# Performance work log

Hardware: AMD Instinct MI355X
Metric: run time of the kernel (lower is better)

## Reference

```python
import jax, jax.numpy as jnp
import numpy as np

N = 50000      # nodes
E = 800000     # edges (before self-loops)
G = 64         # graphs in batch
IN, HID, OUT, H = 128, 64, 64, 4
NEG_SLOPE = 0.2
BN_EPS = 1e-5


def setup_inputs() -> dict:
    key = jax.random.key(0)
    ks = jax.random.split(key, 16)
    s = 0.1
    return {
        "x": jax.random.normal(ks[0], (N, IN), jnp.float32),
        "edge_index": jax.random.randint(ks[1], (2, E), 0, N, dtype=jnp.int64),
        "batch": jnp.sort(jax.random.randint(ks[2], (N,), 0, G, dtype=jnp.int64)),
        "num_graphs": G,
        "W1": jax.random.normal(ks[3], (IN, H * HID), jnp.float32) * s,
        "att_src1": jax.random.normal(ks[4], (H, HID), jnp.float32) * s,
        "att_dst1": jax.random.normal(ks[5], (H, HID), jnp.float32) * s,
        "b1": jnp.zeros((HID,), jnp.float32),
        "W2": jax.random.normal(ks[6], (HID, H * OUT), jnp.float32) * s,
        "att_src2": jax.random.normal(ks[7], (H, OUT), jnp.float32) * s,
        "att_dst2": jax.random.normal(ks[8], (H, OUT), jnp.float32) * s,
        "b2": jnp.zeros((OUT,), jnp.float32),
        "gate_w1": jax.random.normal(ks[9], (OUT, OUT), jnp.float32) * s,
        "gate_b1": jnp.zeros((OUT,), jnp.float32),
        "bn_gamma": jnp.ones((OUT,), jnp.float32),
        "bn_beta": jnp.zeros((OUT,), jnp.float32),
        "gate_w2": jax.random.normal(ks[10], (OUT, 1), jnp.float32) * s,
        "gate_b2": jnp.zeros((1,), jnp.float32),
        "lin_w": jax.random.normal(ks[11], (OUT, 1), jnp.float32) * s,
        "lin_b": jnp.zeros((1,), jnp.float32),
    }


def segment_softmax(e, seg, num_segments):
    # numerically stable softmax over segments (per-destination / per-graph)
    m = jax.ops.segment_max(e, seg, num_segments=num_segments)
    m = jnp.where(jnp.isfinite(m), m, 0.0)
    ex = jnp.exp(e - m[seg])
    den = jax.ops.segment_sum(ex, seg, num_segments=num_segments)
    return ex / (den[seg] + 1e-16)


def gat_conv(x, src, dst, n, W, a_src, a_dst, b, heads, ch):
    h = (x @ W).reshape(n, heads, ch)                 # [N,H,C]
    asrc = jnp.sum(h * a_src, axis=-1)                # [N,H]
    adst = jnp.sum(h * a_dst, axis=-1)                # [N,H]
    e = jax.nn.leaky_relu(asrc[src] + adst[dst], NEG_SLOPE)   # [E',H]
    alpha = segment_softmax(e, dst, n)                # softmax over incoming edges
    out = jax.ops.segment_sum(h[src] * alpha[:, :, None], dst, num_segments=n)
    return jnp.mean(out, axis=1) + b                  # concat=False -> head mean


def reference(x, edge_index, batch, num_graphs, W1, att_src1, att_dst1, b1,
              W2, att_src2, att_dst2, b2, gate_w1, gate_b1, bn_gamma, bn_beta,
              gate_w2, gate_b2, lin_w, lin_b):
    n = x.shape[0]
    loop = jnp.arange(n, dtype=edge_index.dtype)      # PyG add_self_loops default
    src = jnp.concatenate([edge_index[0], loop])
    dst = jnp.concatenate([edge_index[1], loop])

    out = jax.nn.sigmoid(gat_conv(x, src, dst, n, W1, att_src1, att_dst1, b1, H, HID))
    out = jax.nn.sigmoid(gat_conv(out, src, dst, n, W2, att_src2, att_dst2, b2, H, OUT))

    # GlobalAttention pooling; gate_nn = Linear -> BN(eval, rm=0, rv=1) -> ReLU -> Linear
    g = out @ gate_w1 + gate_b1
    g = (g / jnp.sqrt(1.0 + BN_EPS)) * bn_gamma + bn_beta
    g = jax.nn.relu(g) @ gate_w2 + gate_b2            # [N,1]
    gate = segment_softmax(g, batch, num_graphs)      # per-graph softmax
    pooled = jax.ops.segment_sum(gate * out, batch, num_segments=num_graphs)  # [G,OUT]

    return jax.nn.sigmoid(pooled @ lin_w + lin_b)     # [G,1]
```

## Files before the change

kernel.cpp:

```cpp
#include <hip/hip_runtime.h>


constexpr int NN = 50000;
constexpr int EE = 800000;
constexpr int NG = 64;
constexpr float NEG = 0.2f;
constexpr int MT = NN / 16;
constexpr int SLOTS = 64;
constexpr int CH = 16;
constexpr int GB = (MT + 3) / 4;

constexpr int EB_EDGES = 4096;
constexpr int EBN = (EE + EB_EDGES - 1) / EB_EDGES;
constexpr int NBKT = (NN + 255) / 256;
constexpr int CAP = 48;
constexpr int OVFCAP = 8192;

static_assert(NN % 16 == 0, "fused block = 16 nodes");

using bf16x8 = __attribute__((ext_vector_type(8))) __bf16;
using f32x4  = __attribute__((ext_vector_type(4))) float;
using f32x2  = __attribute__((ext_vector_type(2))) float;

__device__ __forceinline__ float wred(float v) {
#pragma unroll
  for (int o = 32; o; o >>= 1) v += __shfl_down(v, o);
  return v;
}
__device__ __forceinline__ float sigmoidf(float v) { return 1.f / (1.f + __expf(-v)); }
__device__ __forceinline__ float lrelu(float v) { return fmaxf(v, NEG * v); }
__device__ __forceinline__ unsigned short f2b(float f) {
  union { float f; unsigned u; } v; v.f = f;
  unsigned r = v.u + 0x7fff + ((v.u >> 16) & 1);
  return (unsigned short)(r >> 16);
}
__device__ __forceinline__ float b2f(unsigned short b) {
  union { unsigned u; float f; } v; v.u = ((unsigned)b) << 16;
  return v.f;
}

__global__ void prep_kernel(const float* __restrict__ W1, const float* __restrict__ W2,
                            const float* __restrict__ gw1, const float* __restrict__ gamma,
                            const int* __restrict__ batch,
                            unsigned short* __restrict__ W1b, unsigned short* __restrict__ W2b,
                            unsigned short* __restrict__ Bg, int* __restrict__ goffs,
                            int* __restrict__ ovf_cnt) {
  int b = blockIdx.x;
  if (b < 128) {
    int idx = b * 256 + threadIdx.x;
    int j = idx & 7, lane = (idx >> 3) & 63, rest = idx >> 9;
    int kc = rest & 3, ntile = rest >> 2;
    W1b[idx] = f2b(W1[(kc * 32 + (lane >> 4) * 8 + j) * 256 + ntile * 16 + (lane & 15)]);
    return;
  }
  if (b < 192) {
    int idx = (b - 128) * 256 + threadIdx.x;
    int j = idx & 7, lane = (idx >> 3) & 63, rest = idx >> 9;
    int kc = rest & 1, ntile = rest >> 1;
    W2b[idx] = f2b(W2[(kc * 32 + (lane >> 4) * 8 + j) * 256 + ntile * 16 + (lane & 15)]);
    return;
  }
  if (b < 208) {
    int idx = (b - 192) * 256 + threadIdx.x;
    int j = idx & 7, lane = (idx >> 3) & 63, rest = idx >> 9;
    int kc = rest & 1, nt = rest >> 1;
    int k = kc * 32 + (lane >> 4) * 8 + j;
    int n = nt * 16 + (lane & 15);
    Bg[idx] = f2b(gw1[k * 64 + n] * gamma[n] * rsqrtf(1.f + 1e-5f));
    return;
  }
  if (threadIdx.x == 0) *ovf_cnt = 0;
  int g = threadIdx.x;
  if (g <= NG) {
    int lo = 0, hi = NN;
    while (lo < hi) {
      int mid = (lo + hi) >> 1;
      if (batch[mid] < g) lo = mid + 1; else hi = mid;
    }
    goffs[g] = lo;
  }
}

template <int KC>
__device__ __forceinline__ void gemm_body(int mt, int lane, const bf16x8* av,
                                          const unsigned short* Bp,
                                          unsigned char* __restrict__ C8,
                                          const float* __restrict__ att_s,
                                          const float* __restrict__ att_d,
                                          float* __restrict__ asrc,
                                          float* __restrict__ adst) {
  int m0 = mt * 16;
  int q = lane >> 4, r = lane & 15;
  f32x4 acc[16] = {};
#pragma unroll
  for (int kc = 0; kc < KC; ++kc) {
#pragma unroll
    for (int nt = 0; nt < 16; ++nt) {
      bf16x8 b = *(const bf16x8*)&Bp[(((unsigned)nt * KC + kc) * 64 + lane) * 8];
      acc[nt] = __builtin_amdgcn_mfma_f32_16x16x32_bf16(av[kc], b, acc[nt], 0, 0, 0);
    }
  }
#pragma unroll
  for (int reg = 0; reg < 4; ++reg) {
    unsigned row = m0 + q * 4 + reg;
    uint4 pk;
    int w;
    w = __builtin_amdgcn_cvt_pk_fp8_f32(acc[0][reg], acc[1][reg], 0, false);
    w = __builtin_amdgcn_cvt_pk_fp8_f32(acc[2][reg], acc[3][reg], w, true);
    pk.x = (unsigned)w;
    w = __builtin_amdgcn_cvt_pk_fp8_f32(acc[4][reg], acc[5][reg], 0, false);
    w = __builtin_amdgcn_cvt_pk_fp8_f32(acc[6][reg], acc[7][reg], w, true);
    pk.y = (unsigned)w;
    w = __builtin_amdgcn_cvt_pk_fp8_f32(acc[8][reg], acc[9][reg], 0, false);
    w = __builtin_amdgcn_cvt_pk_fp8_f32(acc[10][reg], acc[11][reg], w, true);
    pk.z = (unsigned)w;
    w = __builtin_amdgcn_cvt_pk_fp8_f32(acc[12][reg], acc[13][reg], 0, false);
    w = __builtin_amdgcn_cvt_pk_fp8_f32(acc[14][reg], acc[15][reg], w, true);
    pk.w = (unsigned)w;
    *(uint4*)(C8 + (size_t)row * 256 + (unsigned)r * 16) = pk;
  }
  float ps[4][4] = {}, pd[4][4] = {};
#pragma unroll
  for (int head = 0; head < 4; ++head) {
#pragma unroll
    for (int i = 0; i < 4; ++i) {
      float sv = att_s[head * 64 + i * 16 + r];
      float dv = att_d[head * 64 + i * 16 + r];
#pragma unroll
      for (int reg = 0; reg < 4; ++reg) {
        ps[head][reg] += acc[head * 4 + i][reg] * sv;
        pd[head][reg] += acc[head * 4 + i][reg] * dv;
      }
    }
  }
#pragma unroll
  for (int head = 0; head < 4; ++head)
#pragma unroll
    for (int reg = 0; reg < 4; ++reg)
#pragma unroll
      for (int o = 1; o < 16; o <<= 1) {
        ps[head][reg] += __shfl_xor(ps[head][reg], o);
        pd[head][reg] += __shfl_xor(pd[head][reg], o);
      }
  if (r == 0) {
#pragma unroll
    for (int reg = 0; reg < 4; ++reg) {
      int row = m0 + q * 4 + reg;
#pragma unroll
      for (int head = 0; head < 4; ++head) {
        asrc[row * 4 + head] = ps[head][reg];
        adst[row * 4 + head] = pd[head][reg];
      }
    }
  }
}

__global__ void gemm1_build_kernel(const float* __restrict__ x,
                                   const unsigned short* __restrict__ W1b,
                                   unsigned char* __restrict__ C8,
                                   const float* __restrict__ att_s,
                                   const float* __restrict__ att_d,
                                   float* __restrict__ asrc, float* __restrict__ adst,
                                   const int* __restrict__ ei,
                                   unsigned* __restrict__ bins,
                                   int* __restrict__ binCnt,
                                   int* __restrict__ ovf_cnt,
                                   unsigned* __restrict__ ovf) {
  __shared__ union {
    unsigned short B[128 * 256];
    int hist[NBKT];
  } smem;
  int b = blockIdx.x;
  if (b < GB) {
    int wave = threadIdx.x >> 6, lane = threadIdx.x & 63;
    int mt0 = b * 4 + wave;
    int mt = min(mt0, MT - 1);
    int q = lane >> 4, r = lane & 15;
#pragma unroll
    for (int it = 0; it < 16; ++it)
      ((uint4*)smem.B)[it * 256 + threadIdx.x] = ((const uint4*)W1b)[it * 256 + threadIdx.x];
    bf16x8 av[4];
    {
      const float* Arow = x + (size_t)(mt * 16 + r) * 128 + q * 8;
      float4 f0[4], f1[4];
#pragma unroll
      for (int kc = 0; kc < 4; ++kc) {
        f0[kc] = *(const float4*)(Arow + kc * 32);
        f1[kc] = *(const float4*)(Arow + kc * 32 + 4);
      }
#pragma unroll
      for (int kc = 0; kc < 4; ++kc) {
        union { bf16x8 v; unsigned short s[8]; } u;
        u.s[0] = f2b(f0[kc].x); u.s[1] = f2b(f0[kc].y);
        u.s[2] = f2b(f0[kc].z); u.s[3] = f2b(f0[kc].w);
        u.s[4] = f2b(f1[kc].x); u.s[5] = f2b(f1[kc].y);
        u.s[6] = f2b(f1[kc].z); u.s[7] = f2b(f1[kc].w);
        av[kc] = u.v;
      }
    }
    __syncthreads();
    if (mt0 >= MT) return;
    gemm_body<4>(mt, lane, av, smem.B, C8, att_s, att_d, asrc, adst);
    return;
  }
  int hb = b - GB;
  for (int t = threadIdx.x; t < NBKT; t += 256) smem.hist[t] = 0;
  __syncthreads();
  int e0 = hb * EB_EDGES + threadIdx.x * 16;
#pragma unroll
  for (int k4 = 0; k4 < 4; ++k4) {
    int e = e0 + k4 * 4;
    if (e >= EE) break;
    int4 s4 = *(const int4*)&ei[e];
    int4 d4 = *(const int4*)&ei[EE + e];
    int ss[4] = {s4.x, s4.y, s4.z, s4.w};
    int dd[4] = {d4.x, d4.y, d4.z, d4.w};
#pragma unroll
    for (int u = 0; u < 4; ++u) {
      if (e + u >= EE) break;
      int src = ss[u], dst = dd[u];
      int bkt = dst >> 8;
      int rr = atomicAdd(&smem.hist[bkt], 1);
      if (rr < CAP) {
        bins[((unsigned)hb * NBKT + bkt) * CAP + rr] =
            (unsigned)src | ((unsigned)(dst & 255) << 16);
      } else {
        int o = atomicAdd(ovf_cnt, 1);
        if (o < OVFCAP) ovf[o] = (unsigned)src | ((unsigned)dst << 16);
      }
    }
  }
  __syncthreads();
  for (int t = threadIdx.x; t < NBKT; t += 256) binCnt[hb * NBKT + t] = smem.hist[t];
}

__global__ __launch_bounds__(1024) void csr_build_kernel(
    const unsigned* __restrict__ bins, const int* __restrict__ binCnt,
    const int* __restrict__ ovf_cnt, const unsigned* __restrict__ ovf,
    unsigned short* __restrict__ csr16, int* __restrict__ cnt) {
  int b = blockIdx.x;
  __shared__ int hist[256];
  int t = threadIdx.x;
  int node0 = b << 8;
  if (t < 256) {
    hist[t] = 1;
    int node = node0 + t;
    if (node < NN) csr16[(unsigned)node * SLOTS] = (unsigned short)node;
  }
  __syncthreads();
  int wave = t >> 6, lane = t & 63;
  for (int i = wave; i < EBN; i += 16) {
    int c = binCnt[i * NBKT + b];
    if (c > CAP) c = CAP;
    for (int base = 0; base < c; base += 64) {
      int j = base + lane;
      if (j < c) {
        unsigned p = bins[((unsigned)i * NBKT + b) * CAP + j];
        int dl = p >> 16, src = p & 0xffff;
        int r = atomicAdd(&hist[dl], 1);
        if (r < SLOTS) csr16[(unsigned)(node0 + dl) * SLOTS + r] = (unsigned short)src;
      }
    }
  }
  __syncthreads();
  int oc = *ovf_cnt;
  if (oc > OVFCAP) oc = OVFCAP;
  for (int j = t; j < oc; j += 1024) {
    unsigned p = ovf[j];
    int dst = (int)(p >> 16);
    if ((dst >> 8) == b) {
      int r = atomicAdd(&hist[dst & 255], 1);
      if (r < SLOTS) csr16[(unsigned)dst * SLOTS + r] = (unsigned short)(p & 0xffff);
    }
  }
  __syncthreads();
  if (t < 256) {
    int node = node0 + t;
    if (node < NN) cnt[node] = hist[t];
  }
}

__device__ __forceinline__ float agg_node(int node, int lane,
                                          float* __restrict__ wlds,
                                          float* __restrict__ redw,
                                          const unsigned char* __restrict__ h8,
                                          const float* __restrict__ asrc,
                                          const float* __restrict__ adst,
                                          const int* __restrict__ cnt,
                                          const unsigned short* __restrict__ csr_src) {
  int q4 = lane >> 4, r16 = lane & 15, hgrp = q4;
  int deg = min(cnt[node], SLOTS);
  float adh = adst[node * 4 + hgrp];
  int src_all = csr_src[(unsigned)node * SLOTS + lane];
  float den = 0.f;
#pragma unroll
  for (int i = 0; i < 4; ++i) {
    int slot = i * 16 + r16;
    float w = 0.f;
    if (i * 16 < deg) {
      int s = __shfl(src_all, slot);
      bool valid = slot < deg;
      float xv = asrc[(unsigned)(valid ? s : 0) * 4 + hgrp];
      w = valid ? __expf(lrelu(xv + adh)) : 0.f;
    }
    wlds[slot * 4 + hgrp] = w;
    den += w;
  }
#pragma unroll
  for (int o = 1; o < 16; o <<= 1) den += __shfl_xor(den, o);
  __builtin_amdgcn_wave_barrier();

  const unsigned char* hp = h8 + (unsigned)r16 * 16;
  f32x2 a[8] = {};
#define ACC4(d, wA, wB, wC, wD)                                              \
  {                                                                          \
    a[0] += __builtin_amdgcn_cvt_pk_f32_fp8((d).x, false) * (wA);            \
    a[1] += __builtin_amdgcn_cvt_pk_f32_fp8((d).x, true) * (wA);             \
    a[2] += __builtin_amdgcn_cvt_pk_f32_fp8((d).y, false) * (wB);            \
    a[3] += __builtin_amdgcn_cvt_pk_f32_fp8((d).y, true) * (wB);             \
    a[4] += __builtin_amdgcn_cvt_pk_f32_fp8((d).z, false) * (wC);            \
    a[5] += __builtin_amdgcn_cvt_pk_f32_fp8((d).z, true) * (wC);             \
    a[6] += __builtin_amdgcn_cvt_pk_f32_fp8((d).w, false) * (wD);            \
    a[7] += __builtin_amdgcn_cvt_pk_f32_fp8((d).w, true) * (wD);             \
  }
  int e = 0;
#pragma unroll
  for (int i = 0; i < 4; ++i) {
    if (e >= deg) break;
    int bound = min(deg, (i + 1) * 16);
    if (bound - e == 16) {
      int eq = e + q4;
      int s0 = __shfl(src_all, eq);
      int s1 = __shfl(src_all, eq + 4);
      int s2 = __shfl(src_all, eq + 8);
      int s3 = __shfl(src_all, eq + 12);
      f32x4 w0 = *(const f32x4*)&wlds[(unsigned)eq * 4];
      f32x4 w1 = *(const f32x4*)&wlds[(unsigned)(eq + 4) * 4];
      f32x4 w2 = *(const f32x4*)&wlds[(unsigned)(eq + 8) * 4];
      f32x4 w3 = *(const f32x4*)&wlds[(unsigned)(eq + 12) * 4];
      uint4 d0 = *(const uint4*)(hp + ((unsigned)s0 << 8));
      uint4 d1 = *(const uint4*)(hp + ((unsigned)s1 << 8));
      uint4 d2 = *(const uint4*)(hp + ((unsigned)s2 << 8));
      uint4 d3 = *(const uint4*)(hp + ((unsigned)s3 << 8));
      ACC4(d0, w0[0], w0[1], w0[2], w0[3]);
      ACC4(d1, w1[0], w1[1], w1[2], w1[3]);
      ACC4(d2, w2[0], w2[1], w2[2], w2[3]);
      ACC4(d3, w3[0], w3[1], w3[2], w3[3]);
      e += 16;
    } else {
      for (; e < bound; e += 4) {
        int gg = min(4, bound - e);
        int q4e = min(q4, gg - 1);
        int su = __shfl(src_all, e + q4e);
        f32x4 wv = *(const f32x4*)&wlds[(unsigned)(e + q4e) * 4];
        if (q4 >= gg) { wv[0] = 0.f; wv[1] = 0.f; wv[2] = 0.f; wv[3] = 0.f; }
        uint4 d = *(const uint4*)(hp + ((unsigned)su << 8));
        ACC4(d, wv[0], wv[1], wv[2], wv[3]);
      }
    }
  }
#undef ACC4
  float dh0 = __shfl(den, 0), dh1 = __shfl(den, 16);
  float dh2 = __shfl(den, 32), dh3 = __shfl(den, 48);
  float i0 = 0.25f / (dh0 + 1e-16f), i1 = 0.25f / (dh1 + 1e-16f);
  float i2 = 0.25f / (dh2 + 1e-16f), i3 = 0.25f / (dh3 + 1e-16f);
  f32x4 v0 = {a[0].x * i0, a[0].y * i0, a[1].x * i0, a[1].y * i0};
  f32x4 v1 = {a[2].x * i1, a[2].y * i1, a[3].x * i1, a[3].y * i1};
  f32x4 v2 = {a[4].x * i2, a[4].y * i2, a[5].x * i2, a[5].y * i2};
  f32x4 v3 = {a[6].x * i3, a[6].y * i3, a[7].x * i3, a[7].y * i3};
  float* wb2 = &redw[(unsigned)lane * 16 + (lane & 7) * 4];
  *(f32x4*)(wb2 + 0) = v0;
  *(f32x4*)(wb2 + 4) = v1;
  *(f32x4*)(wb2 + 8) = v2;
  *(f32x4*)(wb2 + 12) = v3;
  __builtin_amdgcn_wave_barrier();
  int base = (lane & 15) * 16 + (lane & 7) * 4 + (lane >> 4);
  float s = 0.f;
#pragma unroll
  for (int q = 0; q < 4; ++q)
#pragma unroll
    for (int h = 0; h < 4; ++h)
      s += redw[q * 256 + base + 4 * h];
  return s;
}

__global__ void agg1_gemm2_kernel(const unsigned char* __restrict__ h8,
                                  const float* __restrict__ asrc1,
                                  const float* __restrict__ adst1,
                                  const int* __restrict__ cnt,
                                  const unsigned short* __restrict__ csr_src,
                                  const float* __restrict__ b1,
                                  const unsigned short* __restrict__ W2b,
                                  const float* __restrict__ as2,
                                  const float* __restrict__ ad2,
                                  unsigned char* __restrict__ h8b,
                                  float* __restrict__ asrc2,
                                  float* __restrict__ adst2) {
  int wv = threadIdx.x >> 6, lane = threadIdx.x & 63;
  __shared__ float wtab[4][256];
  __shared__ union { float red[4][1056]; unsigned ctile[16 * 64]; } sm;
  __shared__ unsigned short A16[16][72];
  for (int nl = 0; nl < 4; ++nl) {
    int rl = wv * 4 + nl;
    int node = blockIdx.x * 16 + rl;
    float s = agg_node(node, lane, wtab[wv], sm.red[wv], h8, asrc1, adst1, cnt, csr_src);
    A16[rl][lane] = f2b(sigmoidf(s + b1[lane]));
  }
  __syncthreads();
  int q = lane >> 4, r = lane & 15;
  bf16x8 a0 = *(const bf16x8*)&A16[r][q * 8];
  bf16x8 a1 = *(const bf16x8*)&A16[r][q * 8 + 32];
  f32x4 acc[4] = {};
#pragma unroll
  for (int ntl = 0; ntl < 4; ++ntl) {
    int ntg = wv * 4 + ntl;
    bf16x8 b0 = *(const bf16x8*)&W2b[(((unsigned)ntg * 2 + 0) * 64 + lane) * 8];
    bf16x8 bq = *(const bf16x8*)&W2b[(((unsigned)ntg * 2 + 1) * 64 + lane) * 8];
    acc[ntl] = __builtin_amdgcn_mfma_f32_16x16x32_bf16(a0, b0, acc[ntl], 0, 0, 0);
    acc[ntl] = __builtin_amdgcn_mfma_f32_16x16x32_bf16(a1, bq, acc[ntl], 0, 0, 0);
  }
  float ps[4] = {}, pd[4] = {};
#pragma unroll
  for (int i = 0; i < 4; ++i) {
    float sv = as2[wv * 64 + i * 16 + r];
    float dv = ad2[wv * 64 + i * 16 + r];
#pragma unroll
    for (int reg = 0; reg < 4; ++reg) {
      ps[reg] += acc[i][reg] * sv;
      pd[reg] += acc[i][reg] * dv;
    }
  }
#pragma unroll
  for (int reg = 0; reg < 4; ++reg)
#pragma unroll
    for (int o = 1; o < 16; o <<= 1) {
      ps[reg] += __shfl_xor(ps[reg], o);
      pd[reg] += __shfl_xor(pd[reg], o);
    }
  if (r == 0) {
#pragma unroll
    for (int reg = 0; reg < 4; ++reg) {
      int row = blockIdx.x * 16 + q * 4 + reg;
      asrc2[row * 4 + wv] = ps[reg];
      adst2[row * 4 + wv] = pd[reg];
    }
  }
#pragma unroll
  for (int reg = 0; reg < 4; ++reg) {
    int rowl = q * 4 + reg;
    int w = __builtin_amdgcn_cvt_pk_fp8_f32(acc[0][reg], acc[1][reg], 0, false);
    w = __builtin_amdgcn_cvt_pk_fp8_f32(acc[2][reg], acc[3][reg], w, true);
    sm.ctile[rowl * 64 + r * 4 + wv] = (unsigned)w;
  }
  __syncthreads();
  int row = threadIdx.x >> 4, seg = threadIdx.x & 15;
  uint4 v = *(const uint4*)&sm.ctile[row * 64 + seg * 4];
  *(uint4*)(h8b + ((size_t)(blockIdx.x * 16 + row)) * 256 + (unsigned)seg * 16) = v;
}

__global__ void aggregate_kernel(const unsigned char* __restrict__ h8,
                                 const float* __restrict__ asrc,
                                 const float* __restrict__ adst,
                                 const int* __restrict__ cnt,
                                 const unsigned short* __restrict__ csr_src,
                                 const float* __restrict__ bias,
                                 unsigned short* __restrict__ outb) {
  int wave = threadIdx.x >> 6, lane = threadIdx.x & 63;
  int node = blockIdx.x * 4 + wave;
  __shared__ float wtab[4][256];
  __shared__ float red[4][1056];
  float s = agg_node(node, lane, wtab[wave], red[wave], h8, asrc, adst, cnt, csr_src);
  float ov = sigmoidf(s + bias[lane]);
  outb[(size_t)node * 64 + lane] = f2b(ov);
}

__global__ void pool_partial_kernel(const int* __restrict__ goffs,
                                    const unsigned short* __restrict__ out2b,
                                    const unsigned short* __restrict__ Bg,
                                    const float* __restrict__ gb1,
                                    const float* __restrict__ gamma,
                                    const float* __restrict__ beta,
                                    const float* __restrict__ gw2,
                                    const float* __restrict__ gb2,
                                    float* __restrict__ part_acc,
                                    float* __restrict__ part_den) {
  int b = blockIdx.x, j = blockIdx.y;
  int beg = goffs[b], end = goffs[b + 1];
  int chunk = (end - beg + CH - 1) / CH;
  int cb = beg + j * chunk;
  int ce = min(end, cb + chunk);
  int lane = threadIdx.x & 63, wave = threadIdx.x >> 6;
  int q = lane >> 4, r = lane & 15;
  const float s = rsqrtf(1.f + 1e-5f);
  float gb2v = gb2[0];
  float accv = 0.f, den = 0.f;
  for (int n0 = cb + wave * 16; n0 < ce; n0 += 64) {
    f32x4 acc[4] = {};
    int row = n0 + r;
    if (row >= NN) row = NN - 1;
    const unsigned short* Arow = out2b + (size_t)row * 64 + q * 8;
#pragma unroll
    for (int kc = 0; kc < 2; ++kc) {
      bf16x8 a = *(const bf16x8*)(Arow + kc * 32);
#pragma unroll
      for (int nt = 0; nt < 4; ++nt) {
        bf16x8 b8 = *(const bf16x8*)&Bg[(((size_t)nt * 2 + kc) * 64 + lane) * 8];
        acc[nt] = __builtin_amdgcn_mfma_f32_16x16x32_bf16(a, b8, acc[nt], 0, 0, 0);
      }
    }
    float sum[4] = {0.f, 0.f, 0.f, 0.f};
#pragma unroll
    for (int nt = 0; nt < 4; ++nt) {
      int col = nt * 16 + r;
      float off = gb1[col] * gamma[col] * s + beta[col];
      float w2 = gw2[col];
#pragma unroll
      for (int reg = 0; reg < 4; ++reg)
        sum[reg] += fmaxf(acc[nt][reg] + off, 0.f) * w2;
    }
#pragma unroll
    for (int reg = 0; reg < 4; ++reg)
#pragma unroll
      for (int o = 1; o < 16; o <<= 1) sum[reg] += __shfl_xor(sum[reg], o);
    float gx[4];
#pragma unroll
    for (int reg = 0; reg < 4; ++reg) {
      int n = n0 + q * 4 + reg;
      gx[reg] = (n < ce) ? __expf(sum[reg] + gb2v) : 0.f;
    }
#pragma unroll
    for (int t = 0; t < 16; ++t) {
      int n = n0 + t;
      if (n >= ce) break;
      float gv = __shfl(gx[t & 3], (t >> 2) << 4);
      accv += gv * b2f(out2b[(size_t)n * 64 + lane]);
      den += gv;
    }
  }
  __shared__ float sacc[4][64];
  __shared__ float sden[4];
  sacc[wave][lane] = accv;
  if (lane == 0) sden[wave] = den;
  __syncthreads();
  if (wave == 0) {
    float a = sacc[0][lane] + sacc[1][lane] + sacc[2][lane] + sacc[3][lane];
    part_acc[((size_t)b * CH + j) * 64 + lane] = a;
    if (lane == 0) part_den[b * CH + j] = sden[0] + sden[1] + sden[2] + sden[3];
  }
}

__global__ void pool_final_kernel(const float* __restrict__ part_acc,
                                  const float* __restrict__ part_den,
                                  const float* __restrict__ lw, const float* __restrict__ lb,
                                  float* __restrict__ out) {
  int b = blockIdx.x, lane = threadIdx.x;
  float a = 0.f;
#pragma unroll
  for (int j = 0; j < CH; ++j) a += part_acc[((size_t)b * CH + j) * 64 + lane];
  float den = (lane < CH) ? part_den[b * CH + lane] : 0.f;
  den = wred(den);
  den = __shfl(den, 0);
  float p = a / (den + 1e-16f);
  float v = wred(p * lw[lane]);
  if (lane == 0) out[b] = sigmoidf(v + lb[0]);
}

extern "C" void kernel_launch(void* const* d_in, const int* in_sizes, int n_in,
                              void* d_out, int out_size, void* d_ws, size_t ws_size,
                              hipStream_t stream) {
  const float* x    = (const float*)d_in[0];
  const int*   ei   = (const int*)d_in[1];
  const int*   batch= (const int*)d_in[2];
  const float* W1   = (const float*)d_in[4];
  const float* as1  = (const float*)d_in[5];
  const float* ad1  = (const float*)d_in[6];
  const float* b1   = (const float*)d_in[7];
  const float* W2   = (const float*)d_in[8];
  const float* as2  = (const float*)d_in[9];
  const float* ad2  = (const float*)d_in[10];
  const float* b2   = (const float*)d_in[11];
  const float* gw1  = (const float*)d_in[12];
  const float* gb1  = (const float*)d_in[13];
  const float* gamma= (const float*)d_in[14];
  const float* beta = (const float*)d_in[15];
  const float* gw2  = (const float*)d_in[16];
  const float* gb2  = (const float*)d_in[17];
  const float* lw   = (const float*)d_in[18];
  const float* lb   = (const float*)d_in[19];
  float* out = (float*)d_out;

  char* ws = (char*)d_ws;
  size_t off = 0;
  auto alloc = [&](size_t bytes) -> void* {
    void* p = ws + off;
    off = (off + bytes + 255) & ~(size_t)255;
    return p;
  };
  unsigned short* W1b    = (unsigned short*)alloc((size_t)128 * 256 * 2);
  unsigned short* W2b    = (unsigned short*)alloc((size_t)64 * 256 * 2);
  unsigned short* Bg     = (unsigned short*)alloc((size_t)64 * 64 * 2);
  unsigned char*  h8     = (unsigned char*)alloc((size_t)NN * 256);
  unsigned char*  h8b    = (unsigned char*)alloc((size_t)NN * 256);
  unsigned short* out2b  = (unsigned short*)alloc((size_t)NN * 64 * 2);
  float*    asrc    = (float*)alloc((size_t)NN * 4 * 4);
  float*    adst    = (float*)alloc((size_t)NN * 4 * 4);
  float*    asrc2   = (float*)alloc((size_t)NN * 4 * 4);
  float*    adst2   = (float*)alloc((size_t)NN * 4 * 4);
  int*      cnt     = (int*)alloc((size_t)NN * 4);
  unsigned short* csr16 = (unsigned short*)alloc((size_t)NN * SLOTS * 2);
  unsigned* bins    = (unsigned*)alloc((size_t)EBN * NBKT * CAP * 4);
  int*      binCnt  = (int*)alloc((size_t)EBN * NBKT * 4);
  int*      ovf_cnt = (int*)alloc(256);
  unsigned* ovf     = (unsigned*)alloc((size_t)OVFCAP * 4);
  int*      goffs   = (int*)alloc((size_t)(NG + 1) * 4);
  float*    pacc    = (float*)alloc((size_t)NG * CH * 64 * 4);
  float*    pden    = (float*)alloc((size_t)NG * CH * 4);

  prep_kernel<<<209, 256, 0, stream>>>(W1, W2, gw1, gamma, batch,
                                       W1b, W2b, Bg, goffs, ovf_cnt);

  gemm1_build_kernel<<<GB + EBN, 256, 0, stream>>>(x, W1b, h8, as1, ad1, asrc, adst,
                                                   ei, bins, binCnt, ovf_cnt, ovf);
  csr_build_kernel<<<NBKT, 1024, 0, stream>>>(bins, binCnt, ovf_cnt, ovf, csr16, cnt);

  agg1_gemm2_kernel<<<MT, 256, 0, stream>>>(h8, asrc, adst, cnt, csr16, b1,
                                            W2b, as2, ad2, h8b, asrc2, adst2);

  aggregate_kernel<<<NN / 4, 256, 0, stream>>>(h8b, asrc2, adst2, cnt, csr16, b2, out2b);

  pool_partial_kernel<<<dim3(NG, CH), 256, 0, stream>>>(goffs, out2b, Bg, gb1, gamma, beta,
                                                        gw2, gb2, pacc, pden);
  pool_final_kernel<<<NG, 64, 0, stream>>>(pacc, pden, lw, lb, out);
}
```

Baseline: 239.0 us.

## Reshuffle CSR build across kernels and fuse pool final via last-block reduction

Moves the edge-binning pass into the prep kernel and merges the CSR bin-scatter into the GEMM1 kernel as extra blocks. The pool partial and final kernels become one, with the last block, found through an atomic counter, doing the final reduction. This cuts two kernel launches and the serialized gaps between them. In exchange the CSR scatter now runs at 256 threads per block instead of 1024, it adds a memset and relies on threadfence ordering, and prep and GEMM1 blocks become uneven.

```diff
diff --git a/kernel.cpp b/kernel.cpp
--- a/kernel.cpp
+++ b/kernel.cpp
@@ -17,6 +17,7 @@
 constexpr int OVFCAP = 8192;
 
 static_assert(NN % 16 == 0, "fused block = 16 nodes");
+static_assert(CAP <= 64, "csr bin scan assumes one 64-lane round");
 
 using bf16x8 = __attribute__((ext_vector_type(8))) __bf16;
 using f32x4  = __attribute__((ext_vector_type(4))) float;
@@ -44,7 +45,10 @@
                             const int* __restrict__ batch,
                             unsigned short* __restrict__ W1b, unsigned short* __restrict__ W2b,
                             unsigned short* __restrict__ Bg, int* __restrict__ goffs,
-                            int* __restrict__ ovf_cnt) {
+                            const int* __restrict__ ei,
+                            unsigned* __restrict__ bins, int* __restrict__ binCnt,
+                            int* __restrict__ ovf_cnt, unsigned* __restrict__ ovf) {
+  __shared__ int hist[NBKT];
   int b = blockIdx.x;
   if (b < 128) {
     int idx = b * 256 + threadIdx.x;
@@ -69,16 +73,47 @@
     Bg[idx] = f2b(gw1[k * 64 + n] * gamma[n] * rsqrtf(1.f + 1e-5f));
     return;
   }
-  if (threadIdx.x == 0) *ovf_cnt = 0;
-  int g = threadIdx.x;
-  if (g <= NG) {
-    int lo = 0, hi = NN;
-    while (lo < hi) {
-      int mid = (lo + hi) >> 1;
-      if (batch[mid] < g) lo = mid + 1; else hi = mid;
-    }
-    goffs[g] = lo;
-  }
+  if (b == 208) {
+    int g = threadIdx.x;
+    if (g <= NG) {
+      int lo = 0, hi = NN;
+      while (lo < hi) {
+        int mid = (lo + hi) >> 1;
+        if (batch[mid] < g) lo = mid + 1; else hi = mid;
+      }
+      goffs[g] = lo;
+    }
+    return;
+  }
+  int hb = b - 209;
+  for (int t = threadIdx.x; t < NBKT; t += 256) hist[t] = 0;
+  __syncthreads();
+  int e0 = hb * EB_EDGES + threadIdx.x * 16;
+#pragma unroll
+  for (int k4 = 0; k4 < 4; ++k4) {
+    int e = e0 + k4 * 4;
+    if (e >= EE) break;
+    int4 s4 = *(const int4*)&ei[e];
+    int4 d4 = *(const int4*)&ei[EE + e];
+    int ss[4] = {s4.x, s4.y, s4.z, s4.w};
+    int dd[4] = {d4.x, d4.y, d4.z, d4.w};
+#pragma unroll
+    for (int u = 0; u < 4; ++u) {
+      if (e + u >= EE) break;
+      int src = ss[u], dst = dd[u];
+      int bkt = dst >> 8;
+      int rr = atomicAdd(&hist[bkt], 1);
+      if (rr < CAP) {
+        bins[((unsigned)hb * NBKT + bkt) * CAP + rr] =
+            (unsigned)src | ((unsigned)(dst & 255) << 16);
+      } else {
+        int o = atomicAdd(ovf_cnt, 1);
+        if (o < OVFCAP) ovf[o] = (unsigned)src | ((unsigned)dst << 16);
+      }
+    }
+  }
+  __syncthreads();
+  for (int t = threadIdx.x; t < NBKT; t += 256) binCnt[hb * NBKT + t] = hist[t];
 }
 
 template <int KC>
@@ -155,20 +190,21 @@
   }
 }
 
-__global__ void gemm1_build_kernel(const float* __restrict__ x,
-                                   const unsigned short* __restrict__ W1b,
-                                   unsigned char* __restrict__ C8,
-                                   const float* __restrict__ att_s,
-                                   const float* __restrict__ att_d,
-                                   float* __restrict__ asrc, float* __restrict__ adst,
-                                   const int* __restrict__ ei,
-                                   unsigned* __restrict__ bins,
-                                   int* __restrict__ binCnt,
-                                   int* __restrict__ ovf_cnt,
-                                   unsigned* __restrict__ ovf) {
+__global__ void gemm1_csr_kernel(const float* __restrict__ x,
+                                 const unsigned short* __restrict__ W1b,
+                                 unsigned char* __restrict__ C8,
+                                 const float* __restrict__ att_s,
+                                 const float* __restrict__ att_d,
+                                 float* __restrict__ asrc, float* __restrict__ adst,
+                                 const unsigned* __restrict__ bins,
+                                 const int* __restrict__ binCnt,
+                                 const int* __restrict__ ovf_cnt,
+                                 const unsigned* __restrict__ ovf,
+                                 unsigned short* __restrict__ csr16,
+                                 int* __restrict__ cnt) {
   __shared__ union {
     unsigned short B[128 * 256];
-    int hist[NBKT];
+    int hist[256];
   } smem;
   int b = blockIdx.x;
   if (b < GB) {
@@ -204,80 +240,36 @@
     return;
   }
   int hb = b - GB;
-  for (int t = threadIdx.x; t < NBKT; t += 256) smem.hist[t] = 0;
-  __syncthreads();
-  int e0 = hb * EB_EDGES + threadIdx.x * 16;
-#pragma unroll
-  for (int k4 = 0; k4 < 4; ++k4) {
-    int e = e0 + k4 * 4;
-    if (e >= EE) break;
-    int4 s4 = *(const int4*)&ei[e];
-    int4 d4 = *(const int4*)&ei[EE + e];
-    int ss[4] = {s4.x, s4.y, s4.z, s4.w};
-    int dd[4] = {d4.x, d4.y, d4.z, d4.w};
-#pragma unroll
-    for (int u = 0; u < 4; ++u) {
-      if (e + u >= EE) break;
-      int src = ss[u], dst = dd[u];
-      int bkt = dst >> 8;
-      int rr = atomicAdd(&smem.hist[bkt], 1);
-      if (rr < CAP) {
-        bins[((unsigned)hb * NBKT + bkt) * CAP + rr] =
-            (unsigned)src | ((unsigned)(dst & 255) << 16);
-      } else {
-        int o = atomicAdd(ovf_cnt, 1);
-        if (o < OVFCAP) ovf[o] = (unsigned)src | ((unsigned)dst << 16);
-      }
-    }
-  }
-  __syncthreads();
-  for (int t = threadIdx.x; t < NBKT; t += 256) binCnt[hb * NBKT + t] = smem.hist[t];
-}
-
-__global__ __launch_bounds__(1024) void csr_build_kernel(
-    const unsigned* __restrict__ bins, const int* __restrict__ binCnt,
-    const int* __restrict__ ovf_cnt, const unsigned* __restrict__ ovf,
-    unsigned short* __restrict__ csr16, int* __restrict__ cnt) {
-  int b = blockIdx.x;
-  __shared__ int hist[256];
   int t = threadIdx.x;
-  int node0 = b << 8;
-  if (t < 256) {
-    hist[t] = 1;
-    int node = node0 + t;
-    if (node < NN) csr16[(unsigned)node * SLOTS] = (unsigned short)node;
-  }
+  int node0 = hb << 8;
+  smem.hist[t] = 1;
+  int node = node0 + t;
+  if (node < NN) csr16[(unsigned)node * SLOTS] = (unsigned short)node;
   __syncthreads();
   int wave = t >> 6, lane = t & 63;
-  for (int i = wave; i < EBN; i += 16) {
-    int c = binCnt[i * NBKT + b];
+  for (int i = wave; i < EBN; i += 4) {
+    int c = binCnt[i * NBKT + hb];
     if (c > CAP) c = CAP;
-    for (int base = 0; base < c; base += 64) {
-      int j = base + lane;
-      if (j < c) {
-        unsigned p = bins[((unsigned)i * NBKT + b) * CAP + j];
-        int dl = p >> 16, src = p & 0xffff;
-        int r = atomicAdd(&hist[dl], 1);
-        if (r < SLOTS) csr16[(unsigned)(node0 + dl) * SLOTS + r] = (unsigned short)src;
-      }
+    if (lane < c) {
+      unsigned p = bins[((unsigned)i * NBKT + hb) * CAP + lane];
+      int dl = p >> 16, src = p & 0xffff;
+      int r = atomicAdd(&smem.hist[dl], 1);
+      if (r < SLOTS) csr16[(unsigned)(node0 + dl) * SLOTS + r] = (unsigned short)src;
     }
   }
   __syncthreads();
   int oc = *ovf_cnt;
   if (oc > OVFCAP) oc = OVFCAP;
-  for (int j = t; j < oc; j += 1024) {
+  for (int j = t; j < oc; j += 256) {
     unsigned p = ovf[j];
     int dst = (int)(p >> 16);
-    if ((dst >> 8) == b) {
-      int r = atomicAdd(&hist[dst & 255], 1);
+    if ((dst >> 8) == hb) {
+      int r = atomicAdd(&smem.hist[dst & 255], 1);
       if (r < SLOTS) csr16[(unsigned)dst * SLOTS + r] = (unsigned short)(p & 0xffff);
     }
   }
   __syncthreads();
-  if (t < 256) {
-    int node = node0 + t;
-    if (node < NN) cnt[node] = hist[t];
-  }
+  if (node < NN) cnt[node] = smem.hist[t];
 }
 
 __device__ __forceinline__ float agg_node(int node, int lane,
@@ -474,16 +466,20 @@
   outb[(size_t)node * 64 + lane] = f2b(ov);
 }
 
-__global__ void pool_partial_kernel(const int* __restrict__ goffs,
-                                    const unsigned short* __restrict__ out2b,
-                                    const unsigned short* __restrict__ Bg,
-                                    const float* __restrict__ gb1,
-                                    const float* __restrict__ gamma,
-                                    const float* __restrict__ beta,
-                                    const float* __restrict__ gw2,
-                                    const float* __restrict__ gb2,
-                                    float* __restrict__ part_acc,
-                                    float* __restrict__ part_den) {
+__global__ void pool_kernel(const int* __restrict__ goffs,
+                            const unsigned short* __restrict__ out2b,
+                            const unsigned short* __restrict__ Bg,
+                            const float* __restrict__ gb1,
+                            const float* __restrict__ gamma,
+                            const float* __restrict__ beta,
+                            const float* __restrict__ gw2,
+                            const float* __restrict__ gb2,
+                            const float* __restrict__ lw,
+                            const float* __restrict__ lb,
+                            float* __restrict__ part_acc,
+                            float* __restrict__ part_den,
+                            int* __restrict__ done,
+                            float* __restrict__ out) {
   int b = blockIdx.x, j = blockIdx.y;
   int beg = goffs[b], end = goffs[b + 1];
   int chunk = (end - beg + CH - 1) / CH;
@@ -547,22 +543,24 @@
     part_acc[((size_t)b * CH + j) * 64 + lane] = a;
     if (lane == 0) part_den[b * CH + j] = sden[0] + sden[1] + sden[2] + sden[3];
   }
-}
-
-__global__ void pool_final_kernel(const float* __restrict__ part_acc,
-                                  const float* __restrict__ part_den,
-                                  const float* __restrict__ lw, const float* __restrict__ lb,
-                                  float* __restrict__ out) {
-  int b = blockIdx.x, lane = threadIdx.x;
-  float a = 0.f;
-#pragma unroll
-  for (int j = 0; j < CH; ++j) a += part_acc[((size_t)b * CH + j) * 64 + lane];
-  float den = (lane < CH) ? part_den[b * CH + lane] : 0.f;
-  den = wred(den);
-  den = __shfl(den, 0);
-  float p = a / (den + 1e-16f);
-  float v = wred(p * lw[lane]);
-  if (lane == 0) out[b] = sigmoidf(v + lb[0]);
+  __threadfence();
+  __shared__ int lastFlag;
+  if (threadIdx.x == 0)
+    lastFlag = (atomicAdd(done, 1) == NG * CH - 1) ? 1 : 0;
+  __syncthreads();
+  if (!lastFlag) return;
+  __threadfence();
+  for (int g = wave; g < NG; g += 4) {
+    float a = 0.f;
+#pragma unroll
+    for (int jj = 0; jj < CH; ++jj) a += part_acc[((size_t)g * CH + jj) * 64 + lane];
+    float dn = (lane < CH) ? part_den[g * CH + lane] : 0.f;
+    dn = wred(dn);
+    dn = __shfl(dn, 0);
+    float p = a / (dn + 1e-16f);
+    float v = wred(p * lw[lane]);
+    if (lane == 0) out[g] = sigmoidf(v + lb[0]);
+  }
 }
 
 extern "C" void kernel_launch(void* const* d_in, const int* in_sizes, int n_in,
@@ -610,25 +608,27 @@
   unsigned short* csr16 = (unsigned short*)alloc((size_t)NN * SLOTS * 2);
   unsigned* bins    = (unsigned*)alloc((size_t)EBN * NBKT * CAP * 4);
   int*      binCnt  = (int*)alloc((size_t)EBN * NBKT * 4);
-  int*      ovf_cnt = (int*)alloc(256);
+  int*      ctrs    = (int*)alloc(256);
   unsigned* ovf     = (unsigned*)alloc((size_t)OVFCAP * 4);
   int*      goffs   = (int*)alloc((size_t)(NG + 1) * 4);
   float*    pacc    = (float*)alloc((size_t)NG * CH * 64 * 4);
   float*    pden    = (float*)alloc((size_t)NG * CH * 4);
 
-  prep_kernel<<<209, 256, 0, stream>>>(W1, W2, gw1, gamma, batch,
-                                       W1b, W2b, Bg, goffs, ovf_cnt);
-
-  gemm1_build_kernel<<<GB + EBN, 256, 0, stream>>>(x, W1b, h8, as1, ad1, asrc, adst,
-                                                   ei, bins, binCnt, ovf_cnt, ovf);
-  csr_build_kernel<<<NBKT, 1024, 0, stream>>>(bins, binCnt, ovf_cnt, ovf, csr16, cnt);
+  hipMemsetAsync(ctrs, 0, 256, stream);
+
+  prep_kernel<<<209 + EBN, 256, 0, stream>>>(W1, W2, gw1, gamma, batch,
+                                             W1b, W2b, Bg, goffs,
+                                             ei, bins, binCnt, ctrs, ovf);
+
+  gemm1_csr_kernel<<<GB + NBKT, 256, 0, stream>>>(x, W1b, h8, as1, ad1, asrc, adst,
+                                                  bins, binCnt, ctrs, ovf, csr16, cnt);
 
   agg1_gemm2_kernel<<<MT, 256, 0, stream>>>(h8, asrc, adst, cnt, csr16, b1,
                                             W2b, as2, ad2, h8b, asrc2, adst2);
 
   aggregate_kernel<<<NN / 4, 256, 0, stream>>>(h8b, asrc2, adst2, cnt, csr16, b2, out2b);
 
-  pool_partial_kernel<<<dim3(NG, CH), 256, 0, stream>>>(goffs, out2b, Bg, gb1, gamma, beta,
-                                                        gw2, gb2, pacc, pden);
-  pool_final_kernel<<<NG, 64, 0, stream>>>(pacc, pden, lw, lb, out);
-}
+  pool_kernel<<<dim3(NG, CH), 256, 0, stream>>>(goffs, out2b, Bg, gb1, gamma, beta,
+                                                gw2, gb2, lw, lb, pacc, pden,
+                                                ctrs + 16, out);
+}
```

Result: slower. 326.2 us (+36.5%).
